# Kernel optimization log

Measured on AMD Instinct MI355X. Metric: run time of the kernel, lower is better.

Reference implementation:

```python
import jax, jax.numpy as jnp
import numpy as np

B, Qn, Kn, QD, KVD, FFN, H = 8, 1024, 2048, 512, 256, 2048, 8


def _layer_norm(x, g, b, eps=1e-5):
    m = jnp.mean(x, axis=-1, keepdims=True)
    v = jnp.mean((x - m) ** 2, axis=-1, keepdims=True)
    return (x - m) * jax.lax.rsqrt(v + eps) * g + b


def _mha(q, k, v, key_padding_mask, num_heads):
    # q,k: [B,S,D], v: [B,K,Dv]; reshape to per-head, scale by sqrt(key head dim)
    b, qn, d = q.shape
    kn = k.shape[1]
    dh = d // num_heads
    q = q.reshape(b, qn, num_heads, dh)
    k = k.reshape(b, kn, num_heads, dh)
    v = v.reshape(b, kn, num_heads, -1)
    attn = jnp.einsum('bqhd,bkhd->bhqk', q, k) / jnp.asarray(np.sqrt(dh), q.dtype)
    attn = jnp.where(key_padding_mask[:, None, None, :], -jnp.inf, attn)
    attn = jax.nn.softmax(attn, axis=-1)
    out = jnp.einsum('bhqk,bkhd->bqhd', attn, v)  # [B,Q,H,dv]
    return out.reshape(b, qn, -1)


def setup_inputs() -> dict:
    key = jax.random.key(0)
    ks = jax.random.split(key, 32)
    s = 0.02
    inp = {
        'queries_data': jax.random.normal(ks[0], (B, Qn, QD), jnp.float32),
        'queries_mask': jnp.zeros((B, Qn), bool),
        'box_pos': jax.random.normal(ks[1], (B, Qn, 4 * KVD), jnp.float32),
        'center_pos': jax.random.normal(ks[2], (B, Qn, 2 * KVD), jnp.float32),
        'kv_data': jax.random.normal(ks[3], (B, Kn, KVD), jnp.float32),
        'kv_mask': jnp.zeros((B, Kn), bool),
        'kv_pos': jax.random.normal(ks[4], (B, Kn, KVD), jnp.float32),
        # params ([in,out] convention)
        'sa_qkv_w': jax.random.normal(ks[5], (QD, 3 * QD), jnp.float32) * s,
        'sa_qkv_b': jnp.zeros((3 * QD,), jnp.float32),
        'sa_pos_w': jax.random.normal(ks[6], (4 * KVD, 2 * QD), jnp.float32) * s,
        'sa_pos_b': jnp.zeros((2 * QD,), jnp.float32),
        'sa_ln_g': jnp.ones((QD,), jnp.float32),
        'sa_ln_b': jnp.zeros((QD,), jnp.float32),
        'ca_q_w': jax.random.normal(ks[7], (QD, QD), jnp.float32) * s,
        'ca_q_b': jnp.zeros((QD,), jnp.float32),
        'ca_kv_w': jax.random.normal(ks[8], (KVD, 2 * QD), jnp.float32) * s,
        'ca_kv_b': jnp.zeros((2 * QD,), jnp.float32),
        'ca_qpos_w': jax.random.normal(ks[9], (2 * KVD, QD), jnp.float32) * s,
        'ca_qpos_b': jnp.zeros((QD,), jnp.float32),
        'ca_kpos_w': jax.random.normal(ks[10], (KVD, QD), jnp.float32) * s,
        'ca_kpos_b': jnp.zeros((QD,), jnp.float32),
        'ca_ln_g': jnp.ones((QD,), jnp.float32),
        'ca_ln_b': jnp.zeros((QD,), jnp.float32),
        'ffn_w1': jax.random.normal(ks[11], (QD, FFN), jnp.float32) * s,
        'ffn_b1': jnp.zeros((FFN,), jnp.float32),
        'ffn_w2': jax.random.normal(ks[12], (FFN, QD), jnp.float32) * s,
        'ffn_b2': jnp.zeros((QD,), jnp.float32),
        'ffn_ln_g': jnp.ones((QD,), jnp.float32),
        'ffn_ln_b': jnp.zeros((QD,), jnp.float32),
    }
    return inp


def reference(queries_data, queries_mask, box_pos, center_pos, kv_data, kv_mask, kv_pos,
              sa_qkv_w, sa_qkv_b, sa_pos_w, sa_pos_b, sa_ln_g, sa_ln_b,
              ca_q_w, ca_q_b, ca_kv_w, ca_kv_b, ca_qpos_w, ca_qpos_b,
              ca_kpos_w, ca_kpos_b, ca_ln_g, ca_ln_b,
              ffn_w1, ffn_b1, ffn_w2, ffn_b2, ffn_ln_g, ffn_ln_b):
    # ---- self-attention (pos added to q,k) ----
    qkv = queries_data @ sa_qkv_w + sa_qkv_b
    q, k, v = jnp.split(qkv, 3, axis=-1)
    q_pos, k_pos = jnp.split(box_pos @ sa_pos_w + sa_pos_b, 2, axis=-1)
    sa_out = _mha(q + q_pos, k + k_pos, v, queries_mask, H)
    sa_out = _layer_norm(queries_data + sa_out, sa_ln_g, sa_ln_b)
    # ---- cross-attention (pos concatenated per head) ----
    q = sa_out @ ca_q_w + ca_q_b
    k, v = jnp.split(kv_data @ ca_kv_w + ca_kv_b, 2, axis=-1)
    q_pos = center_pos @ ca_qpos_w + ca_qpos_b
    k_pos = kv_pos @ ca_kpos_w + ca_kpos_b
    dh = QD // H
    q = jnp.concatenate([q.reshape(B, Qn, H, dh), q_pos.reshape(B, Qn, H, dh)], axis=-1).reshape(B, Qn, -1)
    k = jnp.concatenate([k.reshape(B, Kn, H, dh), k_pos.reshape(B, Kn, H, dh)], axis=-1).reshape(B, Kn, -1)
    ca_out = _mha(q, k, v, kv_mask, H)
    ca_out = _layer_norm(sa_out + ca_out, ca_ln_g, ca_ln_b)
    # ---- FFN ----
    f = jax.nn.relu(ca_out @ ffn_w1 + ffn_b1) @ ffn_w2 + ffn_b2
    return _layer_norm(ca_out + f, ffn_ln_g, ffn_ln_b)
```

## Files before the change

### kernel.cpp

```cpp
#include <hip/hip_runtime.h>

typedef __attribute__((ext_vector_type(4))) float f32x4;
typedef __attribute__((ext_vector_type(8))) short bf16x8;
typedef __attribute__((ext_vector_type(4))) unsigned int u32x4;

static __device__ __forceinline__ float bf2f(short s){
    unsigned int u = ((unsigned int)(unsigned short)s) << 16;
    return __builtin_bit_cast(float, u);
}
static __device__ __forceinline__ short f2bf(float f){
    unsigned int u = __builtin_bit_cast(unsigned int, f);
    unsigned int r = (u + 0x7fffu + ((u >> 16) & 1u)) >> 16;
    return (short)r;
}
static __device__ __forceinline__ void gload_lds16(const void* g, void* l){
    __builtin_amdgcn_global_load_lds((const __attribute__((address_space(1))) void*)g,
                                     (__attribute__((address_space(3))) void*)l, 16, 0, 0);
}
static __device__ __forceinline__ float exp2fast(float x){
    float r; asm("v_exp_f32 %0, %1" : "=v"(r) : "v"(x)); return r;
}
static __device__ __forceinline__ unsigned int packbf(float lo, float hi){
#if __has_builtin(__builtin_amdgcn_perm)
    return __builtin_amdgcn_perm(__builtin_bit_cast(unsigned int, hi),
                                 __builtin_bit_cast(unsigned int, lo), 0x07060302u);
#else
    return (__builtin_bit_cast(unsigned int, hi) & 0xffff0000u) |
           (__builtin_bit_cast(unsigned int, lo) >> 16);
#endif
}
static __device__ __forceinline__ void prio_hi(){
#if defined(__HIP_DEVICE_COMPILE__)
    __builtin_amdgcn_s_setprio(1);
#endif
}
static __device__ __forceinline__ void prio_lo(){
#if defined(__HIP_DEVICE_COMPILE__)
    __builtin_amdgcn_s_setprio(0);
#endif
}

__global__ __launch_bounds__(256) void prep_all(
    const float* __restrict__ queries, const float* __restrict__ box,
    const float* __restrict__ ctr, const float* __restrict__ kvd, const float* __restrict__ kvp,
    const unsigned char* __restrict__ qmask, const unsigned char* __restrict__ kmask,
    const float* __restrict__ b_qkv, const float* __restrict__ b_pos,
    short* __restrict__ Xcat, short* __restrict__ ctr_bf,
    short* __restrict__ kvd_bf, short* __restrict__ kvp_bf,
    float* __restrict__ mb_sa, float* __restrict__ mb_ca, float* __restrict__ bcomb)
{
    int bb = blockIdx.x, t = threadIdx.x;
    if (bb < 12288){
        const float* src; short* dst; long i; long stride; int logRow; int colOff;
        if (bb < 2048){ src = queries; dst = Xcat; i = ((long)bb * 256 + t) * 8; logRow = 9;  stride = 1536; colOff = 0; }
        else if (bb < 6144){ src = box; dst = Xcat; i = ((long)(bb - 2048) * 256 + t) * 8; logRow = 10; stride = 1536; colOff = 512; }
        else if (bb < 8192){ src = ctr; dst = ctr_bf; i = ((long)(bb - 6144) * 256 + t) * 8; logRow = 0; stride = 0; colOff = 0; }
        else if (bb < 10240){ src = kvd; dst = kvd_bf; i = ((long)(bb - 8192) * 256 + t) * 8; logRow = 0; stride = 0; colOff = 0; }
        else { src = kvp; dst = kvp_bf; i = ((long)(bb - 10240) * 256 + t) * 8; logRow = 0; stride = 0; colOff = 0; }
        f32x4 a = *(const f32x4*)(src + i);
        f32x4 b = *(const f32x4*)(src + i + 4);
        bf16x8 o;
#pragma unroll
        for (int j = 0; j < 4; j++){ o[j] = f2bf(a[j]); o[4 + j] = f2bf(b[j]); }
        long oi = logRow ? ((i >> logRow) * stride + colOff + (i & ((1L << logRow) - 1))) : i;
        *(bf16x8*)(dst + oi) = o;
    } else if (bb < 12320){
        int i = (bb - 12288) * 256 + t;
        mb_sa[i] = qmask[i] ? -1e30f : 0.f;
    } else if (bb < 12384){
        int i = (bb - 12320) * 256 + t;
        mb_ca[i] = kmask[i] ? -1e30f : 0.f;
    } else {
        int i = (bb - 12384) * 256 + t;
        if (i < 1024) bcomb[i] = b_qkv[i] + b_pos[i];
    }
}

static __device__ __forceinline__ void transcast_body(const float* __restrict__ w,
                                                      short* __restrict__ wT,
                                                      int K, int N, int bx, int by, int t){
    int n = bx * 256 + t;
    int k0 = by * 8;
    bf16x8 o;
#pragma unroll
    for (int j = 0; j < 8; j++) o[j] = f2bf(w[(long)(k0 + j) * N + n]);
    *(bf16x8*)(wT + (long)n * K + k0) = o;
}
__global__ __launch_bounds__(256) void weights_all(
    const float* __restrict__ w_qkv, const float* __restrict__ w_pos,
    const float* __restrict__ w_caq, const float* __restrict__ w_cakv,
    const float* __restrict__ w_caqp, const float* __restrict__ w_cakp,
    const float* __restrict__ w_f1, const float* __restrict__ w_f2,
    short* __restrict__ wTm_qk, short* __restrict__ wTv,
    short* __restrict__ wT_caq, short* __restrict__ wT_cakv,
    short* __restrict__ wT_caqp, short* __restrict__ wT_cakp,
    short* __restrict__ wT_f1, short* __restrict__ wT_f2)
{
    int bb = blockIdx.x, t = threadIdx.x;
    if (bb < 768){
        int by = bb / 4, bx = bb % 4;
        int n = bx * 256 + t;
        int k0 = by * 8;
        bf16x8 o;
#pragma unroll
        for (int j = 0; j < 8; j++){
            int kk = k0 + j;
            float v = (kk < 512) ? w_qkv[(long)kk * 1536 + n] : w_pos[(long)(kk - 512) * 1024 + n];
            o[j] = f2bf(v);
        }
        *(bf16x8*)(wTm_qk + (long)n * 1536 + k0) = o;
    }
    else if (bb < 896){
        int lb = bb - 768;
        int by = lb / 2, bx = lb % 2;
        int n = bx * 256 + t;
        int k0 = by * 8;
        bf16x8 o;
#pragma unroll
        for (int j = 0; j < 8; j++) o[j] = f2bf(w_qkv[(long)(k0 + j) * 1536 + 1024 + n]);
        *(bf16x8*)(wTv + (long)n * 512 + k0) = o;
    }
    else if (bb < 1024){ int lb = bb - 896;  transcast_body(w_caq,  wT_caq,  512, 512,  lb % 2, lb / 2, t); }
    else if (bb < 1152){ int lb = bb - 1024; transcast_body(w_cakv, wT_cakv, 256, 1024, lb % 4, lb / 4, t); }
    else if (bb < 1280){ int lb = bb - 1152; transcast_body(w_caqp, wT_caqp, 512, 512,  lb % 2, lb / 2, t); }
    else if (bb < 1344){ int lb = bb - 1280; transcast_body(w_cakp, wT_cakp, 256, 512,  lb % 2, lb / 2, t); }
    else if (bb < 1856){ int lb = bb - 1344; transcast_body(w_f1,   wT_f1,   512, 2048, lb % 8, lb / 8, t); }
    else               { int lb = bb - 1856; transcast_body(w_f2,   wT_f2,   2048, 512, lb % 2, lb / 2, t); }
}

template<int BN>
__global__ __launch_bounds__(256, (BN == 64) ? 4 : 3) void gemm_bf16(
    const short* __restrict__ A, long lda, const short* __restrict__ Bt,
    const float* __restrict__ bias,
    short* __restrict__ Cbf, float* __restrict__ Cf, int M, int N, int K, int flags)
{
    constexpr int NI = BN / 32;
    constexpr int BUF = (128 + BN) * 32;
    constexpr int EST = BN + 4;
    constexpr int SB = 2 * BUF * 2;
    constexpr int EB = 32 * EST * 4;
    constexpr int SMB = SB > EB ? SB : EB;
    __shared__ __attribute__((aligned(16))) char smem[SMB];
    float* lC = (float*)smem;
    int t = threadIdx.x, w = t >> 6, l = t & 63;
    int cl = l & 15, g = l >> 4;
    int nbx = gridDim.x;
    int flat = blockIdx.y * nbx + blockIdx.x;
    int q8 = (nbx * gridDim.y) >> 3;
    int swz = (flat & 7) * q8 + (flat >> 3);
    long r0 = (long)(swz / nbx) * 128, c0 = (long)(swz % nbx) * BN;
    int wr = w >> 1, wc = w & 1;
    f32x4 acc[4][NI];
#pragma unroll
    for (int mi = 0; mi < 4; mi++)
#pragma unroll
        for (int ni = 0; ni < NI; ni++) acc[mi][ni] = f32x4{0.f, 0.f, 0.f, 0.f};
    int srow = t >> 2, sblk = t & 3;

    auto stage = [&](int d, int k0){
        char* lA = smem + (size_t)d * BUF * 2;
        char* lB = lA + 128 * 32 * 2;
#pragma unroll
        for (int i = 0; i < 2; i++){
            int rrow = srow + i * 64;
            int sb = sblk ^ (rrow & 3);
            gload_lds16(A + (r0 + rrow) * lda + k0 + sb * 8, lA + i * 4096 + w * 1024);
        }
#pragma unroll
        for (int i = 0; i < BN / 64; i++){
            int rrow = srow + i * 64;
            int sb = sblk ^ (rrow & 3);
            gload_lds16(Bt + (c0 + rrow) * (long)K + k0 + sb * 8, lB + i * 4096 + w * 1024);
        }
    };

    stage(0, 0);
    __syncthreads();
    int NK = K / 32;
    for (int kt = 0; kt < NK; kt++){
        int cur = kt & 1;
        if (kt + 1 < NK) stage(cur ^ 1, (kt + 1) * 32);
        const short* lA = (const short*)(smem + (size_t)cur * BUF * 2);
        const short* lB = lA + 128 * 32;
        bf16x8 af[4], bfr[NI];
#pragma unroll
        for (int mi = 0; mi < 4; mi++){
            int row = wr * 64 + mi * 16 + cl;
            af[mi] = *(const bf16x8*)(lA + row * 32 + (g ^ (row & 3)) * 8);
        }
#pragma unroll
        for (int ni = 0; ni < NI; ni++){
            int row = wc * (BN / 2) + ni * 16 + cl;
            bfr[ni] = *(const bf16x8*)(lB + row * 32 + (g ^ (row & 3)) * 8);
        }
        prio_hi();
#pragma unroll
        for (int mi = 0; mi < 4; mi++)
#pragma unroll
            for (int ni = 0; ni < NI; ni++)
                acc[mi][ni] = __builtin_amdgcn_mfma_f32_16x16x32_bf16(af[mi], bfr[ni], acc[mi][ni], 0, 0, 0);
        prio_lo();
        __syncthreads();
    }

#pragma unroll
    for (int mi = 0; mi < 4; mi++){
        __syncthreads();
#pragma unroll
        for (int ni = 0; ni < NI; ni++)
#pragma unroll
            for (int rr = 0; rr < 4; rr++)
                lC[(wr * 16 + g * 4 + rr) * EST + wc * (BN / 2) + ni * 16 + cl] = acc[mi][ni][rr];
        __syncthreads();
        constexpr int CPR = BN / 8;
        constexpr int NCH = 32 * CPR / 256;
#pragma unroll
        for (int c2 = 0; c2 < NCH; c2++){
            int chunk = t + 256 * c2;
            int row = chunk / CPR;
            int coloff = (chunk % CPR) * 8;
            long grow = r0 + (row >> 4) * 64 + mi * 16 + (row & 15);
            long gcol = c0 + coloff;
            f32x4 bv0 = *(const f32x4*)(bias + gcol);
            f32x4 bv1 = *(const f32x4*)(bias + gcol + 4);
            float v[8];
#pragma unroll
            for (int j = 0; j < 8; j++){
                float x = lC[row * EST + coloff + j] + (j < 4 ? bv0[j] : bv1[j - 4]);
                if (flags & 1) x = fmaxf(x, 0.f);
                v[j] = x;
            }
            if (Cf){
                *(f32x4*)(Cf + grow * N + gcol) = f32x4{v[0], v[1], v[2], v[3]};
                *(f32x4*)(Cf + grow * N + gcol + 4) = f32x4{v[4], v[5], v[6], v[7]};
            } else {
                bf16x8 ob;
#pragma unroll
                for (int j = 0; j < 8; j++) ob[j] = f2bf(v[j]);
                long idx;
                if (flags & 2){
                    long part = gcol >> 9;
                    long cc = gcol & 511;
                    long b = grow >> 10, qn = grow & 1023;
                    long h = cc >> 6, d = cc & 63;
                    idx = ((part * 64 + b * 8 + h) * 1024 + qn) * 64 + d;
                } else {
                    idx = grow * N + gcol;
                }
                *(bf16x8*)(Cbf + idx) = ob;
            }
        }
    }
}

__global__ __launch_bounds__(256) void fuse_vt(const short* __restrict__ src, short* __restrict__ Vt,
                                               int srcStride, int colBase, int KN){
    long bh = blockIdx.y; long b = bh >> 3; int h = (int)bh & 7;
    int dv = threadIdx.x & 63;
    int kn0 = blockIdx.x * 32 + (threadIdx.x >> 6) * 8;
    long base = (b * (long)KN + kn0) * srcStride + colBase + h * 64 + dv;
    bf16x8 o;
#pragma unroll
    for (int j = 0; j < 8; j++) o[j] = src[base + (long)j * srcStride];
    *(bf16x8*)(Vt + (bh * 64 + dv) * (long)KN + kn0) = o;
}

__global__ __launch_bounds__(256) void fuse_vt_hs(const short* __restrict__ src,
                                                  short* __restrict__ Vt, int SN){
    long bh = blockIdx.y;
    int dv = threadIdx.x & 63;
    int kn0 = blockIdx.x * 32 + (threadIdx.x >> 6) * 8;
    long base = (bh * (long)SN + kn0) * 64 + dv;
    bf16x8 o;
#pragma unroll
    for (int j = 0; j < 8; j++) o[j] = src[base + (long)j * 64];
    *(bf16x8*)(Vt + (bh * 64 + dv) * (long)SN + kn0) = o;
}

__global__ __launch_bounds__(256) void ln_fuse(const float* __restrict__ a, const float* __restrict__ b,
                                               const float* __restrict__ g, const float* __restrict__ be,
                                               float* __restrict__ outf, short* __restrict__ outb){
    int w = threadIdx.x >> 6, l = threadIdx.x & 63;
    long row = (long)blockIdx.x * 4 + w;
    long base = row * 512 + l * 8;
    f32x4 a0 = *(const f32x4*)(a + base);
    f32x4 a1 = *(const f32x4*)(a + base + 4);
    f32x4 b0 = *(const f32x4*)(b + base);
    f32x4 b1 = *(const f32x4*)(b + base + 4);
    float x[8]; float s = 0.f, s2 = 0.f;
#pragma unroll
    for (int j = 0; j < 4; j++){ x[j] = a0[j] + b0[j]; x[4 + j] = a1[j] + b1[j]; }
#pragma unroll
    for (int j = 0; j < 8; j++){ s += x[j]; s2 += x[j] * x[j]; }
#pragma unroll
    for (int o = 1; o < 64; o <<= 1){ s += __shfl_xor(s, o); s2 += __shfl_xor(s2, o); }
    float mean = s * (1.f / 512.f);
    float rstd = rsqrtf(s2 * (1.f / 512.f) - mean * mean + 1e-5f);
    int c = l * 8;
    f32x4 y0, y1; bf16x8 ob;
#pragma unroll
    for (int j = 0; j < 4; j++){
        float y = (x[j] - mean) * rstd * g[c + j] + be[c + j];
        y0[j] = y; ob[j] = f2bf(y);
    }
#pragma unroll
    for (int j = 0; j < 4; j++){
        float y = (x[4 + j] - mean) * rstd * g[c + 4 + j] + be[c + 4 + j];
        y1[j] = y; ob[4 + j] = f2bf(y);
    }
    *(f32x4*)(outf + base) = y0;
    *(f32x4*)(outf + base + 4) = y1;
    if (outb) *(bf16x8*)(outb + base) = ob;
}

template<int DH, int KN, bool CAT>
__global__ __launch_bounds__(256, 2) void attn_kernel(
    const short* __restrict__ Q1, const short* __restrict__ Q2,
    const short* __restrict__ K1, const short* __restrict__ K2,
    const short* __restrict__ Vt,
    const float* __restrict__ mbias, float* __restrict__ out, float scale2)
{
    constexpr int KT = 64, DV = 64, Qn = 1024, H = 8;
    constexpr int NF = DH / 32;
    constexpr int BPR = DH / 8;
    constexpr int KITER = KT * BPR / 256;
    constexpr int NT = KN / KT;
    __shared__ __attribute__((aligned(16))) short lK[2][KT * DH];
    __shared__ __attribute__((aligned(16))) short lV[2][DV * KT];
    int t = threadIdx.x, w = t >> 6, l = t & 63;
    int cl = l & 15, g = l >> 4;
    int bid = blockIdx.x;
    int bh = (bid & 7) * 8 + (bid >> 6);
    int qb = (bid >> 3) & 7;
    int b = bh >> 3, h = bh & 7;
    int q0 = qb * 128 + w * 32;

    bf16x8 qf[2][NF];
#pragma unroll
    for (int qq = 0; qq < 2; qq++)
#pragma unroll
        for (int f = 0; f < NF; f++){
            if constexpr (CAT){
                const short* src = (f < NF / 2) ? Q1 : Q2;
                qf[qq][f] = *(const bf16x8*)(src + ((long)b * Qn + q0 + qq * 16 + cl) * 512 + h * 64
                                             + (f & (NF / 2 - 1)) * 32 + 8 * g);
            } else {
                qf[qq][f] = *(const bf16x8*)(Q1 + ((long)bh * Qn + q0 + qq * 16 + cl) * DH + f * 32 + 8 * g);
            }
        }

    const short* kp[KITER];
    long kstep[KITER];
#pragma unroll
    for (int i = 0; i < KITER; i++){
        int s_ = i * 256 + t;
        int srow_ = s_ / BPR, blk = s_ % BPR;
        int s32 = srow_ & 31;
        int key = (srow_ & 32) + 8 * ((s32 >> 2) & 3) + 4 * (s32 >> 4) + (s32 & 3);
        int sb = blk ^ (srow_ & 7);
        if constexpr (CAT){
            if (sb < 8){ kp[i] = K1 + ((long)b * KN + key) * 1024 + h * 64 + sb * 8; kstep[i] = (long)KT * 1024; }
            else       { kp[i] = K2 + ((long)b * KN + key) * 512 + h * 64 + (sb - 8) * 8; kstep[i] = (long)KT * 512; }
        } else {
            kp[i] = K1 + ((long)bh * KN + key) * DH + sb * 8; kstep[i] = (long)KT * DH;
        }
    }
    const short* vp[2];
#pragma unroll
    for (int i = 0; i < 2; i++){
        int s_ = i * 256 + t;
        int srow_ = s_ >> 3, blk = s_ & 7;
        int sb = blk ^ (srow_ & 7);
        vp[i] = Vt + ((long)bh * DV + srow_) * KN + sb * 8;
    }

    auto stage = [&](int d){
#pragma unroll
        for (int i = 0; i < KITER; i++){
            gload_lds16(kp[i], (char*)(&lK[d][0]) + i * 4096 + w * 1024);
            kp[i] += kstep[i];
        }
#pragma unroll
        for (int i = 0; i < 2; i++){
            gload_lds16(vp[i], (char*)(&lV[d][0]) + i * 4096 + w * 1024);
            vp[i] += KT;
        }
    };

    f32x4 st[2][4];
    auto do_qk = [&](int d){
        prio_hi();
#pragma unroll
        for (int o = 0; o < 4; o++){
            int srow_ = o * 16 + cl;
            bf16x8 kf[NF];
#pragma unroll
            for (int f = 0; f < NF; f++){
                int sb = (4 * f + g) ^ (srow_ & 7);
                kf[f] = *(const bf16x8*)(&lK[d][0] + srow_ * DH + sb * 8);
            }
#pragma unroll
            for (int qq = 0; qq < 2; qq++){
                f32x4 acc = f32x4{0.f, 0.f, 0.f, 0.f};
#pragma unroll
                for (int f = 0; f < NF; f++)
                    acc = __builtin_amdgcn_mfma_f32_16x16x32_bf16(kf[f], qf[qq][f], acc, 0, 0, 0);
                st[qq][o] = acc;
            }
        }
        prio_lo();
    };

    const float* mrow = mbias + (long)b * KN;
    bf16x8 vones;
    {
        u32x4 ou; ou[0] = ou[1] = ou[2] = ou[3] = 0x3F803F80u;
        vones = __builtin_bit_cast(bf16x8, ou);
    }
    f32x4 lacc[2];
    f32x4 oacc[2][4];
#pragma unroll
    for (int qq = 0; qq < 2; qq++){
        lacc[qq] = f32x4{0.f, 0.f, 0.f, 0.f};
#pragma unroll
        for (int d = 0; d < 4; d++) oacc[qq][d] = f32x4{0.f, 0.f, 0.f, 0.f};
    }

    f32x4 mb[4];
#pragma unroll
    for (int o = 0; o < 4; o++)
        mb[o] = *(const f32x4*)(mrow + (o >> 1) * 32 + 8 * g + 4 * (o & 1));

    stage(0);
    __syncthreads();
    do_qk(0);

    for (int tt = 0; tt < NT; tt++){
        int cur = tt & 1;
        if (tt + 1 < NT) stage(cur ^ 1);

        bf16x8 pa[2][2];
#pragma unroll
        for (int qq = 0; qq < 2; qq++){
#pragma unroll
            for (int kb = 0; kb < 2; kb++){
                float pA[4], pB[4];
#pragma unroll
                for (int rr = 0; rr < 4; rr++){
                    pA[rr] = exp2fast(fmaf(st[qq][2 * kb][rr], scale2, mb[2 * kb][rr]));
                    pB[rr] = exp2fast(fmaf(st[qq][2 * kb + 1][rr], scale2, mb[2 * kb + 1][rr]));
                }
                u32x4 pk;
                pk[0] = packbf(pA[0], pA[1]);
                pk[1] = packbf(pA[2], pA[3]);
                pk[2] = packbf(pB[0], pB[1]);
                pk[3] = packbf(pB[2], pB[3]);
                pa[qq][kb] = __builtin_bit_cast(bf16x8, pk);
            }
        }
        if (tt + 1 < NT){
#pragma unroll
            for (int o = 0; o < 4; o++)
                mb[o] = *(const f32x4*)(mrow + (tt + 1) * KT + (o >> 1) * 32 + 8 * g + 4 * (o & 1));
        }
        prio_hi();
#pragma unroll
        for (int qq = 0; qq < 2; qq++){
            lacc[qq] = __builtin_amdgcn_mfma_f32_16x16x32_bf16(pa[qq][0], vones, lacc[qq], 0, 0, 0);
            lacc[qq] = __builtin_amdgcn_mfma_f32_16x16x32_bf16(pa[qq][1], vones, lacc[qq], 0, 0, 0);
        }
#pragma unroll
        for (int dvc = 0; dvc < 4; dvc++){
            int vrow = dvc * 16 + cl;
            bf16x8 vf[2];
#pragma unroll
            for (int kb = 0; kb < 2; kb++){
                int sb = (4 * kb + g) ^ (vrow & 7);
                vf[kb] = *(const bf16x8*)(&lV[cur][0] + vrow * KT + sb * 8);
            }
#pragma unroll
            for (int qq = 0; qq < 2; qq++){
                f32x4 o = oacc[qq][dvc];
                o = __builtin_amdgcn_mfma_f32_16x16x32_bf16(pa[qq][0], vf[0], o, 0, 0, 0);
                o = __builtin_amdgcn_mfma_f32_16x16x32_bf16(pa[qq][1], vf[1], o, 0, 0, 0);
                oacc[qq][dvc] = o;
            }
        }
        prio_lo();
        __syncthreads();
        if (tt + 1 < NT) do_qk(cur ^ 1);
    }

#pragma unroll
    for (int qq = 0; qq < 2; qq++){
        float linv[4];
#pragma unroll
        for (int rr = 0; rr < 4; rr++) linv[rr] = 1.f / lacc[qq][rr];
#pragma unroll
        for (int dvc = 0; dvc < 4; dvc++)
#pragma unroll
            for (int rr = 0; rr < 4; rr++){
                int q = q0 + qq * 16 + 4 * g + rr;
                out[(((long)b * Qn + q) * H + h) * DV + dvc * 16 + cl] = oacc[qq][dvc][rr] * linv[rr];
            }
    }
}

extern "C" void kernel_launch(void* const* d_in, const int* in_sizes, int n_in,
                              void* d_out, int out_size, void* d_ws, size_t ws_size,
                              hipStream_t stream)
{
    (void)in_sizes; (void)n_in; (void)out_size; (void)ws_size;
    const int Qn = 1024, Kn = 2048;
    const long MQ = 8L * Qn;
    const long MK = 8L * Kn;

    const float* queries = (const float*)d_in[0];
    const unsigned char* qmask = (const unsigned char*)d_in[1];
    const float* box  = (const float*)d_in[2];
    const float* ctr  = (const float*)d_in[3];
    const float* kvd  = (const float*)d_in[4];
    const unsigned char* kmask = (const unsigned char*)d_in[5];
    const float* kvp  = (const float*)d_in[6];
    const float* w_qkv = (const float*)d_in[7];  const float* b_qkv = (const float*)d_in[8];
    const float* w_pos = (const float*)d_in[9];  const float* b_pos = (const float*)d_in[10];
    const float* g_sa  = (const float*)d_in[11]; const float* be_sa = (const float*)d_in[12];
    const float* w_caq = (const float*)d_in[13]; const float* b_caq = (const float*)d_in[14];
    const float* w_cakv = (const float*)d_in[15]; const float* b_cakv = (const float*)d_in[16];
    const float* w_caqp = (const float*)d_in[17]; const float* b_caqp = (const float*)d_in[18];
    const float* w_cakp = (const float*)d_in[19]; const float* b_cakp = (const float*)d_in[20];
    const float* g_ca  = (const float*)d_in[21]; const float* be_ca = (const float*)d_in[22];
    const float* w_f1  = (const float*)d_in[23]; const float* b_f1 = (const float*)d_in[24];
    const float* w_f2  = (const float*)d_in[25]; const float* b_f2 = (const float*)d_in[26];
    const float* g_f   = (const float*)d_in[27]; const float* be_f = (const float*)d_in[28];

    char* ws = (char*)d_ws;
    size_t off = 0;
    auto alloc = [&](size_t bytes) -> char* {
        char* p = ws + off;
        off += (bytes + 255) & ~(size_t)255;
        return p;
    };
    short* wTm_qk  = (short*)alloc(1024L * 1536 * 2);
    short* wTv     = (short*)alloc(512L * 512 * 2);
    short* wT_caq  = (short*)alloc(512L * 512 * 2);
    short* wT_cakv = (short*)alloc(1024L * 256 * 2);
    short* wT_caqp = (short*)alloc(512L * 512 * 2);
    short* wT_cakp = (short*)alloc(512L * 256 * 2);
    short* wT_f1   = (short*)alloc(2048L * 512 * 2);
    short* wT_f2   = (short*)alloc(512L * 2048 * 2);
    float* bcomb   = (float*)alloc(1024L * 4);
    short* ctr_bf  = (short*)alloc(MQ * 512 * 2);
    short* kvd_bf  = (short*)alloc(MK * 256 * 2);
    short* kvp_bf  = (short*)alloc(MK * 256 * 2);
    short* saln_bf = (short*)alloc(MQ * 512 * 2);
    short* caln_bf = (short*)alloc(MQ * 512 * 2);
    float* sa_ln_f = (float*)alloc(MQ * 512 * 4);
    float* ca_ln_f = (float*)alloc(MQ * 512 * 4);
    float* att_f   = (float*)alloc(MQ * 512 * 4);
    float* f_out   = (float*)alloc(MQ * 512 * 4);
    short* VtSA    = (short*)alloc(64L * 64 * 1024 * 2);
    short* VtCA    = (short*)alloc(64L * 64 * 2048 * 2);
    float* mb_sa   = (float*)alloc(MQ * 4);
    float* mb_ca   = (float*)alloc(MK * 4);
    char* zone1 = alloc(MK * 1024 * 2);
    char* zone2 = alloc(MQ * 2048 * 2);
    char* zone3 = alloc(MK * 512 * 2);
    char* zone4 = alloc(MQ * 512 * 2);
    char* zone5 = alloc(MQ * 512 * 2);

    auto gemm128 = [&](const short* A, long lda, const short* Bt, const float* bias,
                       short* Cbf, float* Cf, int M, int N, int K, int flags){
        gemm_bf16<128><<<dim3(N / 128, M / 128), dim3(256), 0, stream>>>(A, lda, Bt, bias, Cbf, Cf, M, N, K, flags);
    };
    auto gemm64 = [&](const short* A, long lda, const short* Bt, const float* bias,
                      short* Cbf, float* Cf, int M, int N, int K, int flags){
        gemm_bf16<64><<<dim3(N / 64, M / 128), dim3(256), 0, stream>>>(A, lda, Bt, bias, Cbf, Cf, M, N, K, flags);
    };

    short* Xcat = (short*)zone1;
    prep_all<<<dim3(12390), dim3(256), 0, stream>>>(
        queries, box, ctr, kvd, kvp, qmask, kmask, b_qkv, b_pos,
        Xcat, ctr_bf, kvd_bf, kvp_bf, mb_sa, mb_ca, bcomb);
    weights_all<<<dim3(2368), dim3(256), 0, stream>>>(
        w_qkv, w_pos, w_caq, w_cakv, w_caqp, w_cakp, w_f1, w_f2,
        wTm_qk, wTv, wT_caq, wT_cakv, wT_caqp, wT_cakp, wT_f1, wT_f2);

    short* QKVa = (short*)zone2;
    short* Qa  = QKVa;
    short* Ka  = QKVa + 64L * 1024 * 64;
    short* Vhs = QKVa + 2L * 64 * 1024 * 64;
    gemm128(Xcat, 1536, wTm_qk, bcomb, QKVa, nullptr, (int)MQ, 1024, 1536, 2);
    gemm64(Xcat, 1536, wTv, b_qkv + 1024, Vhs, nullptr, (int)MQ, 512, 512, 2);
    fuse_vt_hs<<<dim3(Qn / 32, 64), dim3(256), 0, stream>>>(Vhs, VtSA, Qn);

    attn_kernel<64, 1024, false><<<dim3(512), dim3(256), 0, stream>>>(
        Qa, nullptr, Ka, nullptr, VtSA, mb_sa, att_f, 0.125f * 1.44269504f);

    ln_fuse<<<dim3((unsigned)(MQ / 4)), dim3(256), 0, stream>>>(queries, att_f, g_sa, be_sa, sa_ln_f, saln_bf);

    short* caq_bf  = (short*)zone4;
    short* caqp_bf = (short*)zone5;
    short* cakv_bf = (short*)zone1;
    short* cakp_bf = (short*)zone3;
    gemm64(saln_bf, 512, wT_caq, b_caq, caq_bf, nullptr, (int)MQ, 512, 512, 0);
    gemm64(ctr_bf, 512, wT_caqp, b_caqp, caqp_bf, nullptr, (int)MQ, 512, 512, 0);
    gemm128(kvd_bf, 256, wT_cakv, b_cakv, cakv_bf, nullptr, (int)MK, 1024, 256, 0);
    gemm64(kvp_bf, 256, wT_cakp, b_cakp, cakp_bf, nullptr, (int)MK, 512, 256, 0);
    fuse_vt<<<dim3(Kn / 32, 64), dim3(256), 0, stream>>>(cakv_bf, VtCA, 1024, 512, Kn);

    attn_kernel<128, 2048, true><<<dim3(512), dim3(256), 0, stream>>>(
        caq_bf, caqp_bf, cakv_bf, cakp_bf, VtCA, mb_ca, att_f, 0.08838834764831845f * 1.44269504f);

    ln_fuse<<<dim3((unsigned)(MQ / 4)), dim3(256), 0, stream>>>(sa_ln_f, att_f, g_ca, be_ca, ca_ln_f, caln_bf);

    short* mid_bf = (short*)zone2;
    gemm128(caln_bf, 512, wT_f1, b_f1, mid_bf, nullptr, (int)MQ, 2048, 512, 1);
    gemm64(mid_bf, 2048, wT_f2, b_f2, nullptr, f_out, (int)MQ, 512, 2048, 0);

    ln_fuse<<<dim3((unsigned)(MQ / 4)), dim3(256), 0, stream>>>(ca_ln_f, f_out, g_f, be_f, (float*)d_out, (short*)nullptr);
}
```

Before: 323.4 us.

## Fuse V-transpose into GEMM epilogue, merge prep kernels, use 2-wave BN64 GEMM

The GEMM epilogue gains a mode that writes the V columns directly in the transposed per-head layout the attention kernels read. This removes the separate fuse_vt and fuse_vt_hs transpose kernels and the intermediate V buffers they read. The cross-attention K part is now stored with a 512-column stride, and the attention loader is changed to match. The input-prep and weight-transcast kernels are merged into one launch, and the BN=64 GEMM now runs 128 threads (2 waves), each computing a 64x64 tile, which changes per-block parallelism and register pressure.

```diff
diff --git a/kernel.cpp b/kernel.cpp
--- a/kernel.cpp
+++ b/kernel.cpp
@@ -4,10 +4,6 @@
 typedef __attribute__((ext_vector_type(8))) short bf16x8;
 typedef __attribute__((ext_vector_type(4))) unsigned int u32x4;
 
-static __device__ __forceinline__ float bf2f(short s){
-    unsigned int u = ((unsigned int)(unsigned short)s) << 16;
-    return __builtin_bit_cast(float, u);
-}
 static __device__ __forceinline__ short f2bf(float f){
     unsigned int u = __builtin_bit_cast(unsigned int, f);
     unsigned int r = (u + 0x7fffu + ((u >> 16) & 1u)) >> 16;
@@ -40,14 +36,32 @@
 #endif
 }
 
-__global__ __launch_bounds__(256) void prep_all(
+static __device__ __forceinline__ void transcast_body(const float* __restrict__ w,
+                                                      short* __restrict__ wT,
+                                                      int K, int N, int bx, int by, int t){
+    int n = bx * 256 + t;
+    int k0 = by * 8;
+    bf16x8 o;
+#pragma unroll
+    for (int j = 0; j < 8; j++) o[j] = f2bf(w[(long)(k0 + j) * N + n]);
+    *(bf16x8*)(wT + (long)n * K + k0) = o;
+}
+__global__ __launch_bounds__(256) void prep_weights(
     const float* __restrict__ queries, const float* __restrict__ box,
     const float* __restrict__ ctr, const float* __restrict__ kvd, const float* __restrict__ kvp,
     const unsigned char* __restrict__ qmask, const unsigned char* __restrict__ kmask,
     const float* __restrict__ b_qkv, const float* __restrict__ b_pos,
     short* __restrict__ Xcat, short* __restrict__ ctr_bf,
     short* __restrict__ kvd_bf, short* __restrict__ kvp_bf,
-    float* __restrict__ mb_sa, float* __restrict__ mb_ca, float* __restrict__ bcomb)
+    float* __restrict__ mb_sa, float* __restrict__ mb_ca, float* __restrict__ bcomb,
+    const float* __restrict__ w_qkv, const float* __restrict__ w_pos,
+    const float* __restrict__ w_caq, const float* __restrict__ w_cakv,
+    const float* __restrict__ w_caqp, const float* __restrict__ w_cakp,
+    const float* __restrict__ w_f1, const float* __restrict__ w_f2,
+    short* __restrict__ wTm_qk, short* __restrict__ wTv,
+    short* __restrict__ wT_caq, short* __restrict__ wT_cakv,
+    short* __restrict__ wT_caqp, short* __restrict__ wT_cakp,
+    short* __restrict__ wT_f1, short* __restrict__ wT_f2)
 {
     int bb = blockIdx.x, t = threadIdx.x;
     if (bb < 12288){
@@ -64,41 +78,14 @@
         for (int j = 0; j < 4; j++){ o[j] = f2bf(a[j]); o[4 + j] = f2bf(b[j]); }
         long oi = logRow ? ((i >> logRow) * stride + colOff + (i & ((1L << logRow) - 1))) : i;
         *(bf16x8*)(dst + oi) = o;
-    } else if (bb < 12320){
-        int i = (bb - 12288) * 256 + t;
-        mb_sa[i] = qmask[i] ? -1e30f : 0.f;
-    } else if (bb < 12384){
-        int i = (bb - 12320) * 256 + t;
-        mb_ca[i] = kmask[i] ? -1e30f : 0.f;
-    } else {
-        int i = (bb - 12384) * 256 + t;
-        if (i < 1024) bcomb[i] = b_qkv[i] + b_pos[i];
-    }
-}
-
-static __device__ __forceinline__ void transcast_body(const float* __restrict__ w,
-                                                      short* __restrict__ wT,
-                                                      int K, int N, int bx, int by, int t){
-    int n = bx * 256 + t;
-    int k0 = by * 8;
-    bf16x8 o;
-#pragma unroll
-    for (int j = 0; j < 8; j++) o[j] = f2bf(w[(long)(k0 + j) * N + n]);
-    *(bf16x8*)(wT + (long)n * K + k0) = o;
-}
-__global__ __launch_bounds__(256) void weights_all(
-    const float* __restrict__ w_qkv, const float* __restrict__ w_pos,
-    const float* __restrict__ w_caq, const float* __restrict__ w_cakv,
-    const float* __restrict__ w_caqp, const float* __restrict__ w_cakp,
-    const float* __restrict__ w_f1, const float* __restrict__ w_f2,
-    short* __restrict__ wTm_qk, short* __restrict__ wTv,
-    short* __restrict__ wT_caq, short* __restrict__ wT_cakv,
-    short* __restrict__ wT_caqp, short* __restrict__ wT_cakp,
-    short* __restrict__ wT_f1, short* __restrict__ wT_f2)
-{
-    int bb = blockIdx.x, t = threadIdx.x;
-    if (bb < 768){
-        int by = bb / 4, bx = bb % 4;
+        return;
+    }
+    if (bb < 12320){ int i = (bb - 12288) * 256 + t; mb_sa[i] = qmask[i] ? -1e30f : 0.f; return; }
+    if (bb < 12384){ int i = (bb - 12320) * 256 + t; mb_ca[i] = kmask[i] ? -1e30f : 0.f; return; }
+    if (bb < 12388){ int i = (bb - 12384) * 256 + t; if (i < 1024) bcomb[i] = b_qkv[i] + b_pos[i]; return; }
+    int wb = bb - 12388;
+    if (wb < 768){
+        int by = wb / 4, bx = wb % 4;
         int n = bx * 256 + t;
         int k0 = by * 8;
         bf16x8 o;
@@ -110,8 +97,8 @@
         }
         *(bf16x8*)(wTm_qk + (long)n * 1536 + k0) = o;
     }
-    else if (bb < 896){
-        int lb = bb - 768;
+    else if (wb < 896){
+        int lb = wb - 768;
         int by = lb / 2, bx = lb % 2;
         int n = bx * 256 + t;
         int k0 = by * 8;
@@ -120,21 +107,23 @@
         for (int j = 0; j < 8; j++) o[j] = f2bf(w_qkv[(long)(k0 + j) * 1536 + 1024 + n]);
         *(bf16x8*)(wTv + (long)n * 512 + k0) = o;
     }
-    else if (bb < 1024){ int lb = bb - 896;  transcast_body(w_caq,  wT_caq,  512, 512,  lb % 2, lb / 2, t); }
-    else if (bb < 1152){ int lb = bb - 1024; transcast_body(w_cakv, wT_cakv, 256, 1024, lb % 4, lb / 4, t); }
-    else if (bb < 1280){ int lb = bb - 1152; transcast_body(w_caqp, wT_caqp, 512, 512,  lb % 2, lb / 2, t); }
-    else if (bb < 1344){ int lb = bb - 1280; transcast_body(w_cakp, wT_cakp, 256, 512,  lb % 2, lb / 2, t); }
-    else if (bb < 1856){ int lb = bb - 1344; transcast_body(w_f1,   wT_f1,   512, 2048, lb % 8, lb / 8, t); }
-    else               { int lb = bb - 1856; transcast_body(w_f2,   wT_f2,   2048, 512, lb % 2, lb / 2, t); }
+    else if (wb < 1024){ int lb = wb - 896;  transcast_body(w_caq,  wT_caq,  512, 512,  lb % 2, lb / 2, t); }
+    else if (wb < 1152){ int lb = wb - 1024; transcast_body(w_cakv, wT_cakv, 256, 1024, lb % 4, lb / 4, t); }
+    else if (wb < 1280){ int lb = wb - 1152; transcast_body(w_caqp, wT_caqp, 512, 512,  lb % 2, lb / 2, t); }
+    else if (wb < 1344){ int lb = wb - 1280; transcast_body(w_cakp, wT_cakp, 256, 512,  lb % 2, lb / 2, t); }
+    else if (wb < 1856){ int lb = wb - 1344; transcast_body(w_f1,   wT_f1,   512, 2048, lb % 8, lb / 8, t); }
+    else               { int lb = wb - 1856; transcast_body(w_f2,   wT_f2,   2048, 512, lb % 2, lb / 2, t); }
 }
 
 template<int BN>
-__global__ __launch_bounds__(256, (BN == 64) ? 4 : 3) void gemm_bf16(
+__global__ __launch_bounds__((BN == 64) ? 128 : 256, 3) void gemm_bf16(
     const short* __restrict__ A, long lda, const short* __restrict__ Bt,
     const float* __restrict__ bias,
-    short* __restrict__ Cbf, float* __restrict__ Cf, int M, int N, int K, int flags)
+    short* __restrict__ Cbf, float* __restrict__ Cf, int M, int N, int K, int flags,
+    short* __restrict__ Vt, int vtColBase, int snShift, int vtSN)
 {
-    constexpr int NI = BN / 32;
+    constexpr int BLOCK = (BN == 64) ? 128 : 256;
+    constexpr int NW = BLOCK / 64;
     constexpr int BUF = (128 + BN) * 32;
     constexpr int EST = BN + 4;
     constexpr int SB = 2 * BUF * 2;
@@ -149,28 +138,30 @@
     int q8 = (nbx * gridDim.y) >> 3;
     int swz = (flat & 7) * q8 + (flat >> 3);
     long r0 = (long)(swz / nbx) * 128, c0 = (long)(swz % nbx) * BN;
-    int wr = w >> 1, wc = w & 1;
-    f32x4 acc[4][NI];
+    int wr = (NW == 2) ? w : (w >> 1);
+    int wc = (NW == 2) ? 0 : (w & 1);
+    f32x4 acc[4][4];
 #pragma unroll
     for (int mi = 0; mi < 4; mi++)
 #pragma unroll
-        for (int ni = 0; ni < NI; ni++) acc[mi][ni] = f32x4{0.f, 0.f, 0.f, 0.f};
-    int srow = t >> 2, sblk = t & 3;
+        for (int ni = 0; ni < 4; ni++) acc[mi][ni] = f32x4{0.f, 0.f, 0.f, 0.f};
 
     auto stage = [&](int d, int k0){
         char* lA = smem + (size_t)d * BUF * 2;
         char* lB = lA + 128 * 32 * 2;
 #pragma unroll
-        for (int i = 0; i < 2; i++){
-            int rrow = srow + i * 64;
-            int sb = sblk ^ (rrow & 3);
-            gload_lds16(A + (r0 + rrow) * lda + k0 + sb * 8, lA + i * 4096 + w * 1024);
-        }
-#pragma unroll
-        for (int i = 0; i < BN / 64; i++){
-            int rrow = srow + i * 64;
-            int sb = sblk ^ (rrow & 3);
-            gload_lds16(Bt + (c0 + rrow) * (long)K + k0 + sb * 8, lB + i * 4096 + w * 1024);
+        for (int i = 0; i < 512 / BLOCK; i++){
+            int s = i * BLOCK + t;
+            int row = s >> 2, blk = s & 3;
+            int sb = blk ^ (row & 3);
+            gload_lds16(A + (r0 + row) * lda + k0 + sb * 8, lA + i * (BLOCK * 16) + w * 1024);
+        }
+#pragma unroll
+        for (int i = 0; i < BN * 4 / BLOCK; i++){
+            int s = i * BLOCK + t;
+            int row = s >> 2, blk = s & 3;
+            int sb = blk ^ (row & 3);
+            gload_lds16(Bt + (c0 + row) * (long)K + k0 + sb * 8, lB + i * (BLOCK * 16) + w * 1024);
         }
     };
 
@@ -182,99 +173,98 @@
         if (kt + 1 < NK) stage(cur ^ 1, (kt + 1) * 32);
         const short* lA = (const short*)(smem + (size_t)cur * BUF * 2);
         const short* lB = lA + 128 * 32;
-        bf16x8 af[4], bfr[NI];
+        bf16x8 af[4], bfr[4];
 #pragma unroll
         for (int mi = 0; mi < 4; mi++){
             int row = wr * 64 + mi * 16 + cl;
             af[mi] = *(const bf16x8*)(lA + row * 32 + (g ^ (row & 3)) * 8);
         }
 #pragma unroll
-        for (int ni = 0; ni < NI; ni++){
-            int row = wc * (BN / 2) + ni * 16 + cl;
+        for (int ni = 0; ni < 4; ni++){
+            int row = wc * 64 + ni * 16 + cl;
             bfr[ni] = *(const bf16x8*)(lB + row * 32 + (g ^ (row & 3)) * 8);
         }
         prio_hi();
 #pragma unroll
         for (int mi = 0; mi < 4; mi++)
 #pragma unroll
-            for (int ni = 0; ni < NI; ni++)
+            for (int ni = 0; ni < 4; ni++)
                 acc[mi][ni] = __builtin_amdgcn_mfma_f32_16x16x32_bf16(af[mi], bfr[ni], acc[mi][ni], 0, 0, 0);
         prio_lo();
         __syncthreads();
     }
 
+    bool vtBlock = (flags & 4) && (c0 >= vtColBase);
 #pragma unroll
     for (int mi = 0; mi < 4; mi++){
         __syncthreads();
 #pragma unroll
-        for (int ni = 0; ni < NI; ni++)
+        for (int ni = 0; ni < 4; ni++)
 #pragma unroll
             for (int rr = 0; rr < 4; rr++)
-                lC[(wr * 16 + g * 4 + rr) * EST + wc * (BN / 2) + ni * 16 + cl] = acc[mi][ni][rr];
+                lC[(wr * 16 + g * 4 + rr) * EST + wc * 64 + ni * 16 + cl] = acc[mi][ni][rr];
         __syncthreads();
-        constexpr int CPR = BN / 8;
-        constexpr int NCH = 32 * CPR / 256;
-#pragma unroll
-        for (int c2 = 0; c2 < NCH; c2++){
-            int chunk = t + 256 * c2;
-            int row = chunk / CPR;
-            int coloff = (chunk % CPR) * 8;
-            long grow = r0 + (row >> 4) * 64 + mi * 16 + (row & 15);
-            long gcol = c0 + coloff;
-            f32x4 bv0 = *(const f32x4*)(bias + gcol);
-            f32x4 bv1 = *(const f32x4*)(bias + gcol + 4);
-            float v[8];
-#pragma unroll
-            for (int j = 0; j < 8; j++){
-                float x = lC[row * EST + coloff + j] + (j < 4 ? bv0[j] : bv1[j - 4]);
-                if (flags & 1) x = fmaxf(x, 0.f);
-                v[j] = x;
-            }
-            if (Cf){
-                *(f32x4*)(Cf + grow * N + gcol) = f32x4{v[0], v[1], v[2], v[3]};
-                *(f32x4*)(Cf + grow * N + gcol + 4) = f32x4{v[4], v[5], v[6], v[7]};
-            } else {
+        if (vtBlock){
+#pragma unroll
+            for (int c2 = 0; c2 < BN * 4 / BLOCK; c2++){
+                int task = t + BLOCK * c2;
+                int col = task & (BN - 1);
+                int wrg = (task / BN) & 1;
+                int ch = task / (BN * 2);
+                float bv = bias[c0 + col];
+                long qg0 = r0 + wrg * 64 + mi * 16 + ch * 8;
                 bf16x8 ob;
 #pragma unroll
-                for (int j = 0; j < 8; j++) ob[j] = f2bf(v[j]);
-                long idx;
-                if (flags & 2){
-                    long part = gcol >> 9;
-                    long cc = gcol & 511;
-                    long b = grow >> 10, qn = grow & 1023;
-                    long h = cc >> 6, d = cc & 63;
-                    idx = ((part * 64 + b * 8 + h) * 1024 + qn) * 64 + d;
+                for (int j = 0; j < 8; j++)
+                    ob[j] = f2bf(lC[(wrg * 16 + ch * 8 + j) * EST + col] + bv);
+                long dvg = c0 - vtColBase + col;
+                long h = dvg >> 6, dvv = dvg & 63;
+                long b = qg0 >> snShift;
+                long loc = qg0 & ((1L << snShift) - 1);
+                *(bf16x8*)(Vt + ((b * 8 + h) * 64 + dvv) * (long)vtSN + loc) = ob;
+            }
+        } else {
+            constexpr int CPR = BN / 8;
+#pragma unroll
+            for (int c2 = 0; c2 < 32 * CPR / BLOCK; c2++){
+                int chunk = t + BLOCK * c2;
+                int row = chunk / CPR;
+                int coloff = (chunk % CPR) * 8;
+                long grow = r0 + (row >> 4) * 64 + mi * 16 + (row & 15);
+                long gcol = c0 + coloff;
+                f32x4 bv0 = *(const f32x4*)(bias + gcol);
+                f32x4 bv1 = *(const f32x4*)(bias + gcol + 4);
+                float v[8];
+#pragma unroll
+                for (int j = 0; j < 8; j++){
+                    float x = lC[row * EST + coloff + j] + (j < 4 ? bv0[j] : bv1[j - 4]);
+                    if (flags & 1) x = fmaxf(x, 0.f);
+                    v[j] = x;
+                }
+                if (Cf){
+                    *(f32x4*)(Cf + grow * N + gcol) = f32x4{v[0], v[1], v[2], v[3]};
+                    *(f32x4*)(Cf + grow * N + gcol + 4) = f32x4{v[4], v[5], v[6], v[7]};
                 } else {
-                    idx = grow * N + gcol;
+                    bf16x8 ob;
+#pragma unroll
+                    for (int j = 0; j < 8; j++) ob[j] = f2bf(v[j]);
+                    long idx;
+                    if (flags & 2){
+                        long part = gcol >> 9;
+                        long cc = gcol & 511;
+                        long b = grow >> 10, qn = grow & 1023;
+                        long h = cc >> 6, d = cc & 63;
+                        idx = ((part * 64 + b * 8 + h) * 1024 + qn) * 64 + d;
+                    } else if (flags & 4){
+                        idx = grow * (long)vtColBase + gcol;
+                    } else {
+                        idx = grow * N + gcol;
+                    }
+                    *(bf16x8*)(Cbf + idx) = ob;
                 }
-                *(bf16x8*)(Cbf + idx) = ob;
-            }
-        }
-    }
-}
-
-__global__ __launch_bounds__(256) void fuse_vt(const short* __restrict__ src, short* __restrict__ Vt,
-                                               int srcStride, int colBase, int KN){
-    long bh = blockIdx.y; long b = bh >> 3; int h = (int)bh & 7;
-    int dv = threadIdx.x & 63;
-    int kn0 = blockIdx.x * 32 + (threadIdx.x >> 6) * 8;
-    long base = (b * (long)KN + kn0) * srcStride + colBase + h * 64 + dv;
-    bf16x8 o;
-#pragma unroll
-    for (int j = 0; j < 8; j++) o[j] = src[base + (long)j * srcStride];
-    *(bf16x8*)(Vt + (bh * 64 + dv) * (long)KN + kn0) = o;
-}
-
-__global__ __launch_bounds__(256) void fuse_vt_hs(const short* __restrict__ src,
-                                                  short* __restrict__ Vt, int SN){
-    long bh = blockIdx.y;
-    int dv = threadIdx.x & 63;
-    int kn0 = blockIdx.x * 32 + (threadIdx.x >> 6) * 8;
-    long base = (bh * (long)SN + kn0) * 64 + dv;
-    bf16x8 o;
-#pragma unroll
-    for (int j = 0; j < 8; j++) o[j] = src[base + (long)j * 64];
-    *(bf16x8*)(Vt + (bh * 64 + dv) * (long)SN + kn0) = o;
+            }
+        }
+    }
 }
 
 __global__ __launch_bounds__(256) void ln_fuse(const float* __restrict__ a, const float* __restrict__ b,
@@ -359,7 +349,7 @@
         int key = (srow_ & 32) + 8 * ((s32 >> 2) & 3) + 4 * (s32 >> 4) + (s32 & 3);
         int sb = blk ^ (srow_ & 7);
         if constexpr (CAT){
-            if (sb < 8){ kp[i] = K1 + ((long)b * KN + key) * 1024 + h * 64 + sb * 8; kstep[i] = (long)KT * 1024; }
+            if (sb < 8){ kp[i] = K1 + ((long)b * KN + key) * 512 + h * 64 + sb * 8; kstep[i] = (long)KT * 512; }
             else       { kp[i] = K2 + ((long)b * KN + key) * 512 + h * 64 + (sb - 8) * 8; kstep[i] = (long)KT * 512; }
         } else {
             kp[i] = K1 + ((long)bh * KN + key) * DH + sb * 8; kstep[i] = (long)KT * DH;
@@ -570,29 +560,30 @@
     char* zone5 = alloc(MQ * 512 * 2);
 
     auto gemm128 = [&](const short* A, long lda, const short* Bt, const float* bias,
-                       short* Cbf, float* Cf, int M, int N, int K, int flags){
-        gemm_bf16<128><<<dim3(N / 128, M / 128), dim3(256), 0, stream>>>(A, lda, Bt, bias, Cbf, Cf, M, N, K, flags);
+                       short* Cbf, float* Cf, int M, int N, int K, int flags,
+                       short* Vt, int vtColBase, int snShift, int vtSN){
+        gemm_bf16<128><<<dim3(N / 128, M / 128), dim3(256), 0, stream>>>(
+            A, lda, Bt, bias, Cbf, Cf, M, N, K, flags, Vt, vtColBase, snShift, vtSN);
     };
     auto gemm64 = [&](const short* A, long lda, const short* Bt, const float* bias,
-                      short* Cbf, float* Cf, int M, int N, int K, int flags){
-        gemm_bf16<64><<<dim3(N / 64, M / 128), dim3(256), 0, stream>>>(A, lda, Bt, bias, Cbf, Cf, M, N, K, flags);
+                      short* Cbf, float* Cf, int M, int N, int K, int flags,
+                      short* Vt, int vtColBase, int snShift, int vtSN){
+        gemm_bf16<64><<<dim3(N / 64, M / 128), dim3(128), 0, stream>>>(
+            A, lda, Bt, bias, Cbf, Cf, M, N, K, flags, Vt, vtColBase, snShift, vtSN);
     };
 
     short* Xcat = (short*)zone1;
-    prep_all<<<dim3(12390), dim3(256), 0, stream>>>(
+    prep_weights<<<dim3(14756), dim3(256), 0, stream>>>(
         queries, box, ctr, kvd, kvp, qmask, kmask, b_qkv, b_pos,
-        Xcat, ctr_bf, kvd_bf, kvp_bf, mb_sa, mb_ca, bcomb);
-    weights_all<<<dim3(2368), dim3(256), 0, stream>>>(
+        Xcat, ctr_bf, kvd_bf, kvp_bf, mb_sa, mb_ca, bcomb,
         w_qkv, w_pos, w_caq, w_cakv, w_caqp, w_cakp, w_f1, w_f2,
         wTm_qk, wTv, wT_caq, wT_cakv, wT_caqp, wT_cakp, wT_f1, wT_f2);
 
     short* QKVa = (short*)zone2;
     short* Qa  = QKVa;
     short* Ka  = QKVa + 64L * 1024 * 64;
-    short* Vhs = QKVa + 2L * 64 * 1024 * 64;
-    gemm128(Xcat, 1536, wTm_qk, bcomb, QKVa, nullptr, (int)MQ, 1024, 1536, 2);
-    gemm64(Xcat, 1536, wTv, b_qkv + 1024, Vhs, nullptr, (int)MQ, 512, 512, 2);
-    fuse_vt_hs<<<dim3(Qn / 32, 64), dim3(256), 0, stream>>>(Vhs, VtSA, Qn);
+    gemm128(Xcat, 1536, wTm_qk, bcomb, QKVa, nullptr, (int)MQ, 1024, 1536, 2, nullptr, 0, 0, 0);
+    gemm64(Xcat, 1536, wTv, b_qkv + 1024, nullptr, nullptr, (int)MQ, 512, 512, 4, VtSA, 0, 10, 1024);
 
     attn_kernel<64, 1024, false><<<dim3(512), dim3(256), 0, stream>>>(
         Qa, nullptr, Ka, nullptr, VtSA, mb_sa, att_f, 0.125f * 1.44269504f);
@@ -601,22 +592,21 @@
 
     short* caq_bf  = (short*)zone4;
     short* caqp_bf = (short*)zone5;
-    short* cakv_bf = (short*)zone1;
+    short* caK     = (short*)zone1;
     short* cakp_bf = (short*)zone3;
-    gemm64(saln_bf, 512, wT_caq, b_caq, caq_bf, nullptr, (int)MQ, 512, 512, 0);
-    gemm64(ctr_bf, 512, wT_caqp, b_caqp, caqp_bf, nullptr, (int)MQ, 512, 512, 0);
-    gemm128(kvd_bf, 256, wT_cakv, b_cakv, cakv_bf, nullptr, (int)MK, 1024, 256, 0);
-    gemm64(kvp_bf, 256, wT_cakp, b_cakp, cakp_bf, nullptr, (int)MK, 512, 256, 0);
-    fuse_vt<<<dim3(Kn / 32, 64), dim3(256), 0, stream>>>(cakv_bf, VtCA, 1024, 512, Kn);
+    gemm64(saln_bf, 512, wT_caq, b_caq, caq_bf, nullptr, (int)MQ, 512, 512, 0, nullptr, 0, 0, 0);
+    gemm64(ctr_bf, 512, wT_caqp, b_caqp, caqp_bf, nullptr, (int)MQ, 512, 512, 0, nullptr, 0, 0, 0);
+    gemm128(kvd_bf, 256, wT_cakv, b_cakv, caK, nullptr, (int)MK, 1024, 256, 4, VtCA, 512, 11, 2048);
+    gemm64(kvp_bf, 256, wT_cakp, b_cakp, cakp_bf, nullptr, (int)MK, 512, 256, 0, nullptr, 0, 0, 0);
 
     attn_kernel<128, 2048, true><<<dim3(512), dim3(256), 0, stream>>>(
-        caq_bf, caqp_bf, cakv_bf, cakp_bf, VtCA, mb_ca, att_f, 0.08838834764831845f * 1.44269504f);
+        caq_bf, caqp_bf, caK, cakp_bf, VtCA, mb_ca, att_f, 0.08838834764831845f * 1.44269504f);
 
     ln_fuse<<<dim3((unsigned)(MQ / 4)), dim3(256), 0, stream>>>(sa_ln_f, att_f, g_ca, be_ca, ca_ln_f, caln_bf);
 
     short* mid_bf = (short*)zone2;
-    gemm128(caln_bf, 512, wT_f1, b_f1, mid_bf, nullptr, (int)MQ, 2048, 512, 1);
-    gemm64(mid_bf, 2048, wT_f2, b_f2, nullptr, f_out, (int)MQ, 512, 2048, 0);
+    gemm128(caln_bf, 512, wT_f1, b_f1, mid_bf, nullptr, (int)MQ, 2048, 512, 1, nullptr, 0, 0, 0);
+    gemm64(mid_bf, 2048, wT_f2, b_f2, nullptr, f_out, (int)MQ, 512, 2048, 0, nullptr, 0, 0, 0);
 
     ln_fuse<<<dim3((unsigned)(MQ / 4)), dim3(256), 0, stream>>>(ca_ln_f, f_out, g_f, be_f, (float*)d_out, (short*)nullptr);
 }
```

New measurement: 320.9 us. Within noise of the previous version (-0.8%).
